# Kernel optimization log

Hardware: AMD Instinct MI355X
Metric: run time of the kernel (lower is better)

The kernel has to match this reference:

```python
import jax, jax.numpy as jnp
import numpy as np
from jax import lax

EPS = 1e-3  # Keras BatchNormalization default epsilon
DN = ('NHWC', 'HWIO', 'NHWC')


def _bn(x, gamma, beta, mean, var):
    inv = gamma * lax.rsqrt(var + EPS)
    return x * inv + (beta - mean * inv)


def setup_inputs() -> dict:
    key = jax.random.key(0)
    ks = jax.random.split(key, 5)
    B, H, W, C = 32, 56, 56, 256
    G, CG = 32, 4  # cardinality, channels per group
    CM = G * CG    # 128 mid channels
    x = jax.random.normal(ks[0], (B, H, W, C), jnp.float32)
    # 32 branch 1x1 convs (256->4 each) stacked -> one 256->128 conv
    w1 = jax.random.normal(ks[1], (1, 1, C, CM), jnp.float32) * 0.05
    b1 = jnp.zeros((CM,), jnp.float32)
    g1 = jnp.ones((CM,), jnp.float32)
    be1 = jnp.zeros((CM,), jnp.float32)
    m1 = jnp.zeros((CM,), jnp.float32)
    v1 = jnp.ones((CM,), jnp.float32)
    # 32 branch 3x3 convs (4->4 each) stacked -> grouped conv kernel [3,3,4,128]
    w2 = jax.random.normal(ks[2], (3, 3, CG, CM), jnp.float32) * 0.1
    b2 = jnp.zeros((CM,), jnp.float32)
    g2 = jnp.ones((CM,), jnp.float32)
    be2 = jnp.zeros((CM,), jnp.float32)
    m2 = jnp.zeros((CM,), jnp.float32)
    v2 = jnp.ones((CM,), jnp.float32)
    # final 1x1 conv 128 -> 256
    w3 = jax.random.normal(ks[3], (1, 1, CM, C), jnp.float32) * 0.05
    b3 = jnp.zeros((C,), jnp.float32)
    return dict(x=x, w1=w1, b1=b1, g1=g1, be1=be1, m1=m1, v1=v1,
                w2=w2, b2=b2, g2=g2, be2=be2, m2=m2, v2=v2,
                w3=w3, b3=b3)


def reference(x, w1, b1, g1, be1, m1, v1, w2, b2, g2, be2, m2, v2, w3, b3):
    # branch 1x1 convs fused: conv 256 -> 128
    h = lax.conv_general_dilated(x, w1, (1, 1), 'SAME', dimension_numbers=DN) + b1
    h = jax.nn.relu(_bn(h, g1, be1, m1, v1))
    # branch 3x3 convs fused: grouped conv, 32 groups of 4 channels
    h = lax.conv_general_dilated(h, w2, (1, 1), 'SAME', dimension_numbers=DN,
                                 feature_group_count=32) + b2
    h = jax.nn.relu(_bn(h, g2, be2, m2, v2))
    # Dropout(0.2) is identity at inference
    # final 1x1 conv 128 -> 256, residual add, relu
    out = lax.conv_general_dilated(h, w3, (1, 1), 'SAME', dimension_numbers=DN) + b3
    return jax.nn.relu(out + x)
```

## Files before the change

kernel.cpp:

```cpp
#include <hip/hip_runtime.h>
#include <stdint.h>

typedef unsigned short u16;
typedef unsigned int   u32;
typedef __attribute__((ext_vector_type(8))) short bf16x8;
typedef __attribute__((ext_vector_type(4))) float f32x4;

#define EPS 1e-3f
#define NB 32
#define HW 56
#define CI 256
#define CM 128
#define PIX (NB*HW*HW)

__device__ __forceinline__ float asf(u32 i){ union{u32 u; float f;} t; t.u=i; return t.f; }
__device__ __forceinline__ u16 f2bf(float f){
  union{float f; u32 u;} t; t.f = f;
  u32 x = t.u;
  return (u16)((x + 0x7fffu + ((x>>16)&1u)) >> 16);
}

__global__ __launch_bounds__(256) void kprep(
    const float* __restrict__ w1, const float* __restrict__ b1, const float* __restrict__ g1,
    const float* __restrict__ be1, const float* __restrict__ m1, const float* __restrict__ v1,
    const float* __restrict__ w2, const float* __restrict__ b2, const float* __restrict__ g2,
    const float* __restrict__ be2, const float* __restrict__ m2, const float* __restrict__ v2,
    const float* __restrict__ w3,
    u16* __restrict__ w1s, u16* __restrict__ w3s, u16* __restrict__ w2s,
    float* __restrict__ A1, float* __restrict__ B1,
    float* __restrict__ A2, float* __restrict__ B2){
  int i = blockIdx.x*256 + threadIdx.x;
  if (i < 32768){
    {
      int j = i & 7, lane = (i >> 3) & 63, kt = (i >> 9) & 7, t = i >> 12;
      int col = lane & 15, quad = lane >> 4;
      int n = t*16 + col, k = kt*32 + quad*8 + j;
      w1s[i] = f2bf(w1[k*CM + n]);
    }
    {
      int j = i & 7, lane = (i >> 3) & 63, kc = (i >> 9) & 3, t = i >> 11;
      int col = lane & 15, quad = lane >> 4;
      int n = t*16 + col, k = kc*32 + quad*8 + j;
      w3s[i] = f2bf(w3[k*CI + n]);
    }
  }
  if (i < 40960){
    int j = i & 7, lane = (i >> 3) & 63;
    int pv = (i >> 9) % 10, t = (i >> 9) / 10;
    int pp = pv % 5; bool lo = pv >= 5;
    int col = lane & 15, quad = lane >> 4;
    int klocal = quad*8 + j;
    int tap = (klocal < 16) ? 2*pp : 2*pp + 1;
    int c = klocal & 15;
    float wv = 0.f;
    if (tap <= 8 && (c >> 2) == (col >> 2))
      wv = w2[(tap*4 + (c & 3))*CM + t*16 + col];
    u16 hi = f2bf(wv);
    if (!lo) w2s[i] = hi;
    else     w2s[i] = f2bf(wv - asf((u32)hi << 16));
  }
  if (i < 128){
    float s1 = g1[i] * rsqrtf(v1[i] + EPS);
    A1[i] = s1;
    B1[i] = b1[i]*s1 + be1[i] - m1[i]*s1;
    float s2 = g2[i] * rsqrtf(v2[i] + EPS);
    A2[i] = s2;
    B2[i] = b2[i]*s2 + be2[i] - m2[i]*s2;
  }
}

#define K1_LS 72
__global__ __launch_bounds__(256) void k1(const float* __restrict__ x,
    const u16* __restrict__ w1s, const float* __restrict__ A1v,
    const float* __restrict__ B1v, u16* __restrict__ h1){
  __shared__ __align__(16) char smem[128*136*2];
  u16* As = (u16*)smem;
  const int tid  = threadIdx.x;
  const int lane = tid & 63, wv = tid >> 6;
  const int col  = lane & 15, quad = lane >> 4;
  const long p0 = (long)blockIdx.x * 128;
  f32x4 acc[8][2];
  #pragma unroll
  for (int a = 0; a < 8; a++)
    #pragma unroll
    for (int b = 0; b < 2; b++){ acc[a][b][0]=0.f; acc[a][b][1]=0.f; acc[a][b][2]=0.f; acc[a][b][3]=0.f; }
  for (int kc = 0; kc < 4; kc++){
    #pragma unroll
    for (int r = 0; r < 8; r++){
      int idx = r*256 + tid;
      int m = idx >> 4, f4 = idx & 15;
      float4 v = *(const float4*)(x + (p0+m)*CI + kc*64 + f4*4);
      u32 lo = (u32)f2bf(v.x) | ((u32)f2bf(v.y) << 16);
      u32 hi = (u32)f2bf(v.z) | ((u32)f2bf(v.w) << 16);
      *(uint2*)(As + m*K1_LS + f4*4) = make_uint2(lo, hi);
    }
    __syncthreads();
    #pragma unroll
    for (int ks = 0; ks < 2; ks++){
      const int kt = kc*2 + ks;
      bf16x8 bfr[2], af[8];
      #pragma unroll
      for (int nt = 0; nt < 2; nt++)
        bfr[nt] = *(const bf16x8*)(w1s + (size_t)(((wv*2+nt)*8 + kt)*64 + lane)*8);
      #pragma unroll
      for (int mt = 0; mt < 8; mt++)
        af[mt] = *(const bf16x8*)(As + (mt*16 + col)*K1_LS + ks*32 + quad*8);
      #pragma unroll
      for (int mt = 0; mt < 8; mt++)
        #pragma unroll
        for (int nt = 0; nt < 2; nt++)
          acc[mt][nt] = __builtin_amdgcn_mfma_f32_16x16x32_bf16(af[mt], bfr[nt], acc[mt][nt], 0, 0, 0);
    }
    __syncthreads();
  }
  u16* outw = (u16*)smem;
  #pragma unroll
  for (int nt = 0; nt < 2; nt++){
    int n = wv*32 + nt*16 + col;
    float a1 = A1v[n], b1v = B1v[n];
    #pragma unroll
    for (int mt = 0; mt < 8; mt++)
      #pragma unroll
      for (int reg = 0; reg < 4; reg++){
        int m = mt*16 + quad*4 + reg;
        outw[m*136 + n] = f2bf(fmaxf(acc[mt][nt][reg]*a1 + b1v, 0.f));
      }
  }
  __syncthreads();
  #pragma unroll
  for (int r = 0; r < 8; r++){
    int idx = r*256 + tid;
    int m = idx >> 4, u4 = idx & 15;
    uint4 v = *(const uint4*)(outw + m*136 + u4*8);
    *(uint4*)(h1 + (p0+m)*CM + u4*8) = v;
  }
}

#define LSH1 136
__global__ __launch_bounds__(512, 2) void k23(const u16* __restrict__ h1,
    const u16* __restrict__ w2s, const float* __restrict__ A2v,
    const float* __restrict__ B2v, const u16* __restrict__ w3s,
    const float* __restrict__ b3, const float* __restrict__ x,
    float* __restrict__ out){
  __shared__ __align__(16) char smem[3*HW*LSH1*2 + 64*256];
  u16*  tile = (u16*)smem;
  char* h2t  = smem + 3*HW*LSH1*2;
  float* pre = (float*)smem;

  const int tid = threadIdx.x;
  const int bid = blockIdx.x;
  const int blk = (bid & 7)*224 + (bid >> 3);
  const int y0 = blk % HW;
  const long p0 = (long)blk * HW;

  #pragma unroll
  for (int r = 0; r < 3; r++){
    const int yy = y0 + r - 1;
    const bool valid = (yy >= 0 && yy < HW);
    const uint4* src = (const uint4*)(h1 + (long)(blk - y0 + yy)*HW*CM);
    for (int i = tid; i < 896; i += 512){
      uint4 v = make_uint4(0u,0u,0u,0u);
      if (valid) v = src[i];
      int px = i >> 4, ch = (i & 15)*8;
      *(uint4*)(tile + (r*HW + px)*LSH1 + ch) = v;
    }
  }
  __syncthreads();

  float4 xr[4];
  #pragma unroll
  for (int it = 0; it < 4; it++){
    int i = tid + it*512;
    if (i < 1792){
      int m = i >> 5, f4 = i & 31;
      xr[it] = *(const float4*)(x + (p0+m)*CI + f4*4);
    }
  }

  const int lane = tid & 63, wv = tid >> 6;
  const int col  = lane & 15, quad = lane >> 4;

  const int mh = wv >> 2, nq = wv & 3;
  f32x4 acc2[2][2];
  #pragma unroll
  for (int a = 0; a < 2; a++)
    #pragma unroll
    for (int b = 0; b < 2; b++){ acc2[a][b][0]=0.f; acc2[a][b][1]=0.f; acc2[a][b][2]=0.f; acc2[a][b][3]=0.f; }
  #pragma unroll
  for (int pp = 0; pp < 5; pp++){
    const int tA = 2*pp, tB = (pp < 4) ? 2*pp + 1 : 8;
    const int dyA = tA/3, dxA = tA%3, dyB = tB/3, dxB = tB%3;
    const int dy = (quad < 2) ? dyA : dyB;
    const int dx = (quad < 2) ? dxA : dxB;
    bf16x8 bh[2], bl[2];
    #pragma unroll
    for (int ntl = 0; ntl < 2; ntl++){
      int nt = nq*2 + ntl;
      bh[ntl] = *(const bf16x8*)(w2s + (size_t)((nt*10 + pp)*64 + lane)*8);
      bl[ntl] = *(const bf16x8*)(w2s + (size_t)((nt*10 + 5 + pp)*64 + lane)*8);
    }
    #pragma unroll
    for (int mtl = 0; mtl < 2; mtl++){
      int px = (mh*2 + mtl)*16 + col;
      int sx = px + dx - 1;
      u32 mk = (px < HW && sx >= 0 && sx < HW) ? 0xffffffffu : 0u;
      int sxc = sx < 0 ? 0 : (sx > 55 ? 55 : sx);
      const u16* abase = tile + (dy*HW + sxc)*LSH1 + (quad & 1)*8;
      #pragma unroll
      for (int ntl = 0; ntl < 2; ntl++){
        int nt = nq*2 + ntl;
        union { bf16x8 v; u32 w[4]; } af;
        af.v = *(const bf16x8*)(abase + nt*16);
        af.w[0] &= mk; af.w[1] &= mk; af.w[2] &= mk; af.w[3] &= mk;
        acc2[mtl][ntl] = __builtin_amdgcn_mfma_f32_16x16x32_bf16(af.v, bh[ntl], acc2[mtl][ntl], 0, 0, 0);
        acc2[mtl][ntl] = __builtin_amdgcn_mfma_f32_16x16x32_bf16(af.v, bl[ntl], acc2[mtl][ntl], 0, 0, 0);
      }
    }
  }
  #pragma unroll
  for (int ntl = 0; ntl < 2; ntl++){
    int co = (nq*2 + ntl)*16 + col;
    float a2 = A2v[co], b2v = B2v[co];
    #pragma unroll
    for (int mtl = 0; mtl < 2; mtl++)
      #pragma unroll
      for (int reg = 0; reg < 4; reg++){
        int m = (mh*2 + mtl)*16 + quad*4 + reg;
        float v = acc2[mtl][ntl][reg]*a2 + b2v;
        u16 hv = (m < HW) ? f2bf(fmaxf(v, 0.f)) : (u16)0;
        *(u16*)(h2t + m*256 + ((co*2) ^ ((m & 7) << 4))) = hv;
      }
  }
  __syncthreads();

  f32x4 acc3[4][2];
  #pragma unroll
  for (int a = 0; a < 4; a++)
    #pragma unroll
    for (int b = 0; b < 2; b++){ acc3[a][b][0]=0.f; acc3[a][b][1]=0.f; acc3[a][b][2]=0.f; acc3[a][b][3]=0.f; }
  float bias[2];
  #pragma unroll
  for (int nt = 0; nt < 2; nt++) bias[nt] = b3[wv*32 + nt*16 + col];
  #pragma unroll
  for (int kc = 0; kc < 4; kc++){
    bf16x8 bfr[2];
    #pragma unroll
    for (int nt = 0; nt < 2; nt++)
      bfr[nt] = *(const bf16x8*)(w3s + (size_t)(((wv*2+nt)*4 + kc)*64 + lane)*8);
    #pragma unroll
    for (int mt = 0; mt < 4; mt++){
      int row = mt*16 + col;
      bf16x8 af = *(const bf16x8*)(h2t + row*256 + ((kc*64 + quad*16) ^ ((row & 7) << 4)));
      #pragma unroll
      for (int nt = 0; nt < 2; nt++)
        acc3[mt][nt] = __builtin_amdgcn_mfma_f32_16x16x32_bf16(af, bfr[nt], acc3[mt][nt], 0, 0, 0);
    }
  }

  if (wv < 4){
    #pragma unroll
    for (int mt = 0; mt < 4; mt++)
      #pragma unroll
      for (int nt = 0; nt < 2; nt++)
        #pragma unroll
        for (int reg = 0; reg < 4; reg++){
          int m = mt*16 + quad*4 + reg;
          pre[m*132 + (wv&3)*32 + nt*16 + col] = acc3[mt][nt][reg] + bias[nt];
        }
  }
  __syncthreads();
  #pragma unroll
  for (int it = 0; it < 4; it++){
    int i = tid + it*512;
    if (i < 1792){
      int m = i >> 5, f4 = i & 31;
      float4 pv = *(const float4*)(pre + m*132 + f4*4);
      float4 o;
      o.x = fmaxf(pv.x + xr[it].x, 0.f);
      o.y = fmaxf(pv.y + xr[it].y, 0.f);
      o.z = fmaxf(pv.z + xr[it].z, 0.f);
      o.w = fmaxf(pv.w + xr[it].w, 0.f);
      *(float4*)(out + (p0+m)*CI + f4*4) = o;
    }
  }
  __syncthreads();

  if (wv >= 4){
    #pragma unroll
    for (int mt = 0; mt < 4; mt++)
      #pragma unroll
      for (int nt = 0; nt < 2; nt++)
        #pragma unroll
        for (int reg = 0; reg < 4; reg++){
          int m = mt*16 + quad*4 + reg;
          pre[m*132 + (wv&3)*32 + nt*16 + col] = acc3[mt][nt][reg] + bias[nt];
        }
  }
  __syncthreads();
  #pragma unroll
  for (int it = 0; it < 4; it++){
    int i = tid + it*512;
    if (i < 1792){
      int m = i >> 5, f4 = i & 31;
      float4 xv = *(const float4*)(x + (p0+m)*CI + 128 + f4*4);
      float4 pv = *(const float4*)(pre + m*132 + f4*4);
      float4 o;
      o.x = fmaxf(pv.x + xv.x, 0.f);
      o.y = fmaxf(pv.y + xv.y, 0.f);
      o.z = fmaxf(pv.z + xv.z, 0.f);
      o.w = fmaxf(pv.w + xv.w, 0.f);
      *(float4*)(out + (p0+m)*CI + 128 + f4*4) = o;
    }
  }
}

extern "C" void kernel_launch(void* const* d_in, const int* in_sizes, int n_in,
                              void* d_out, int out_size, void* d_ws, size_t ws_size,
                              hipStream_t stream){
  (void)in_sizes; (void)n_in; (void)out_size; (void)ws_size;
  const float* x   = (const float*)d_in[0];
  const float* w1  = (const float*)d_in[1];
  const float* b1  = (const float*)d_in[2];
  const float* g1  = (const float*)d_in[3];
  const float* be1 = (const float*)d_in[4];
  const float* m1  = (const float*)d_in[5];
  const float* v1  = (const float*)d_in[6];
  const float* w2  = (const float*)d_in[7];
  const float* b2  = (const float*)d_in[8];
  const float* g2  = (const float*)d_in[9];
  const float* be2 = (const float*)d_in[10];
  const float* m2  = (const float*)d_in[11];
  const float* v2  = (const float*)d_in[12];
  const float* w3  = (const float*)d_in[13];
  const float* b3  = (const float*)d_in[14];

  char* ws = (char*)d_ws;
  u16* h1  = (u16*)ws;
  u16* w1s = (u16*)(ws + (size_t)PIX*CM*2);
  u16* w3s = w1s + 32768;
  float* A1 = (float*)(w3s + 32768);
  float* B1 = A1 + 128;
  float* A2 = B1 + 128;
  float* B2 = A2 + 128;
  u16* w2s = (u16*)(B2 + 128);

  kprep<<<160, 256, 0, stream>>>(w1,b1,g1,be1,m1,v1,w2,b2,g2,be2,m2,v2,w3,
                                 w1s,w3s,w2s,A1,B1,A2,B2);
  k1<<<PIX/128, 256, 0, stream>>>(x, w1s, A1, B1, h1);
  k23<<<NB*HW, 512, 0, stream>>>(h1, w2s, A2, B2, w3s, b3, x, (float*)d_out);
}
```

Baseline: 250.4 us.

## Process two image rows per block in fused grouped-conv and projection kernel

The fused 3x3-grouped-conv plus 1x1-projection kernel now handles two output rows (112 pixels) per block, loading a 4-row halo tile instead of 3 rows per single row. This cuts halo reloads of h1 and amortizes the w2/w3 weight fetches over more pixels, with MFMA tiles filling 7 full 16-row tiles instead of padding 56 to 64. LDS is reused between the input tile, h2 and the output staging buffer to fit the larger tile, which adds barriers and more accumulator registers per thread and may reduce occupancy. The early prefetch of the residual x is dropped, so x is now loaded after the GEMM.

```diff
diff --git a/kernel.cpp b/kernel.cpp
--- a/kernel.cpp
+++ b/kernel.cpp
@@ -142,22 +142,22 @@
     const float* __restrict__ B2v, const u16* __restrict__ w3s,
     const float* __restrict__ b3, const float* __restrict__ x,
     float* __restrict__ out){
-  __shared__ __align__(16) char smem[3*HW*LSH1*2 + 64*256];
+  __shared__ __align__(16) char smem[4*HW*LSH1*2];
   u16*  tile = (u16*)smem;
-  char* h2t  = smem + 3*HW*LSH1*2;
+  char* h2t  = smem;
   float* pre = (float*)smem;
 
   const int tid = threadIdx.x;
   const int bid = blockIdx.x;
-  const int blk = (bid & 7)*224 + (bid >> 3);
-  const int y0 = blk % HW;
-  const long p0 = (long)blk * HW;
-
-  #pragma unroll
-  for (int r = 0; r < 3; r++){
+  const int blk = (bid & 7)*112 + (bid >> 3);
+  const int y0 = (blk % 28) * 2;
+  const long p0 = (long)blk * 112;
+
+  #pragma unroll
+  for (int r = 0; r < 4; r++){
     const int yy = y0 + r - 1;
     const bool valid = (yy >= 0 && yy < HW);
-    const uint4* src = (const uint4*)(h1 + (long)(blk - y0 + yy)*HW*CM);
+    const uint4* src = (const uint4*)(h1 + ((long)p0 + (long)(r-1)*HW)*CM);
     for (int i = tid; i < 896; i += 512){
       uint4 v = make_uint4(0u,0u,0u,0u);
       if (valid) v = src[i];
@@ -167,75 +167,58 @@
   }
   __syncthreads();
 
-  float4 xr[4];
-  #pragma unroll
-  for (int it = 0; it < 4; it++){
-    int i = tid + it*512;
-    if (i < 1792){
-      int m = i >> 5, f4 = i & 31;
-      xr[it] = *(const float4*)(x + (p0+m)*CI + f4*4);
-    }
-  }
-
   const int lane = tid & 63, wv = tid >> 6;
   const int col  = lane & 15, quad = lane >> 4;
 
-  const int mh = wv >> 2, nq = wv & 3;
-  f32x4 acc2[2][2];
-  #pragma unroll
-  for (int a = 0; a < 2; a++)
-    #pragma unroll
-    for (int b = 0; b < 2; b++){ acc2[a][b][0]=0.f; acc2[a][b][1]=0.f; acc2[a][b][2]=0.f; acc2[a][b][3]=0.f; }
+  const int nt2 = wv;
+  f32x4 acc2[7];
+  #pragma unroll
+  for (int a = 0; a < 7; a++){ acc2[a][0]=0.f; acc2[a][1]=0.f; acc2[a][2]=0.f; acc2[a][3]=0.f; }
+  int rbase[7], xq[7];
+  #pragma unroll
+  for (int mt = 0; mt < 7; mt++){
+    int px = mt*16 + col;
+    int rr = (px >= HW) ? 1 : 0;
+    rbase[mt] = rr; xq[mt] = px - rr*HW;
+  }
   #pragma unroll
   for (int pp = 0; pp < 5; pp++){
     const int tA = 2*pp, tB = (pp < 4) ? 2*pp + 1 : 8;
-    const int dyA = tA/3, dxA = tA%3, dyB = tB/3, dxB = tB%3;
-    const int dy = (quad < 2) ? dyA : dyB;
-    const int dx = (quad < 2) ? dxA : dxB;
-    bf16x8 bh[2], bl[2];
-    #pragma unroll
-    for (int ntl = 0; ntl < 2; ntl++){
-      int nt = nq*2 + ntl;
-      bh[ntl] = *(const bf16x8*)(w2s + (size_t)((nt*10 + pp)*64 + lane)*8);
-      bl[ntl] = *(const bf16x8*)(w2s + (size_t)((nt*10 + 5 + pp)*64 + lane)*8);
-    }
-    #pragma unroll
-    for (int mtl = 0; mtl < 2; mtl++){
-      int px = (mh*2 + mtl)*16 + col;
-      int sx = px + dx - 1;
-      u32 mk = (px < HW && sx >= 0 && sx < HW) ? 0xffffffffu : 0u;
+    const int dy = (quad < 2) ? tA/3 : tB/3;
+    const int dx = (quad < 2) ? tA%3 : tB%3;
+    bf16x8 bh = *(const bf16x8*)(w2s + (size_t)((nt2*10 + pp)*64 + lane)*8);
+    bf16x8 bl = *(const bf16x8*)(w2s + (size_t)((nt2*10 + 5 + pp)*64 + lane)*8);
+    #pragma unroll
+    for (int mt = 0; mt < 7; mt++){
+      int sx = xq[mt] + dx - 1;
+      u32 mk = (sx >= 0 && sx < HW) ? 0xffffffffu : 0u;
       int sxc = sx < 0 ? 0 : (sx > 55 ? 55 : sx);
-      const u16* abase = tile + (dy*HW + sxc)*LSH1 + (quad & 1)*8;
-      #pragma unroll
-      for (int ntl = 0; ntl < 2; ntl++){
-        int nt = nq*2 + ntl;
-        union { bf16x8 v; u32 w[4]; } af;
-        af.v = *(const bf16x8*)(abase + nt*16);
-        af.w[0] &= mk; af.w[1] &= mk; af.w[2] &= mk; af.w[3] &= mk;
-        acc2[mtl][ntl] = __builtin_amdgcn_mfma_f32_16x16x32_bf16(af.v, bh[ntl], acc2[mtl][ntl], 0, 0, 0);
-        acc2[mtl][ntl] = __builtin_amdgcn_mfma_f32_16x16x32_bf16(af.v, bl[ntl], acc2[mtl][ntl], 0, 0, 0);
+      const u16* ap = tile + ((rbase[mt]+dy)*HW + sxc)*LSH1 + (quad & 1)*8 + nt2*16;
+      union { bf16x8 v; u32 w[4]; } af;
+      af.v = *(const bf16x8*)ap;
+      af.w[0] &= mk; af.w[1] &= mk; af.w[2] &= mk; af.w[3] &= mk;
+      acc2[mt] = __builtin_amdgcn_mfma_f32_16x16x32_bf16(af.v, bh, acc2[mt], 0, 0, 0);
+      acc2[mt] = __builtin_amdgcn_mfma_f32_16x16x32_bf16(af.v, bl, acc2[mt], 0, 0, 0);
+    }
+  }
+  __syncthreads();
+
+  {
+    float a2 = A2v[nt2*16 + col], b2v = B2v[nt2*16 + col];
+    #pragma unroll
+    for (int mt = 0; mt < 7; mt++)
+      #pragma unroll
+      for (int reg = 0; reg < 4; reg++){
+        int m = mt*16 + quad*4 + reg;
+        u16 hv = f2bf(fmaxf(acc2[mt][reg]*a2 + b2v, 0.f));
+        *(u16*)(h2t + m*256 + (((nt2*16 + col)*2) ^ ((m & 7) << 4))) = hv;
       }
-    }
-  }
-  #pragma unroll
-  for (int ntl = 0; ntl < 2; ntl++){
-    int co = (nq*2 + ntl)*16 + col;
-    float a2 = A2v[co], b2v = B2v[co];
-    #pragma unroll
-    for (int mtl = 0; mtl < 2; mtl++)
-      #pragma unroll
-      for (int reg = 0; reg < 4; reg++){
-        int m = (mh*2 + mtl)*16 + quad*4 + reg;
-        float v = acc2[mtl][ntl][reg]*a2 + b2v;
-        u16 hv = (m < HW) ? f2bf(fmaxf(v, 0.f)) : (u16)0;
-        *(u16*)(h2t + m*256 + ((co*2) ^ ((m & 7) << 4))) = hv;
-      }
-  }
-  __syncthreads();
-
-  f32x4 acc3[4][2];
-  #pragma unroll
-  for (int a = 0; a < 4; a++)
+  }
+  __syncthreads();
+
+  f32x4 acc3[7][2];
+  #pragma unroll
+  for (int a = 0; a < 7; a++)
     #pragma unroll
     for (int b = 0; b < 2; b++){ acc3[a][b][0]=0.f; acc3[a][b][1]=0.f; acc3[a][b][2]=0.f; acc3[a][b][3]=0.f; }
   float bias[2];
@@ -248,7 +231,7 @@
     for (int nt = 0; nt < 2; nt++)
       bfr[nt] = *(const bf16x8*)(w3s + (size_t)(((wv*2+nt)*4 + kc)*64 + lane)*8);
     #pragma unroll
-    for (int mt = 0; mt < 4; mt++){
+    for (int mt = 0; mt < 7; mt++){
       int row = mt*16 + col;
       bf16x8 af = *(const bf16x8*)(h2t + row*256 + ((kc*64 + quad*16) ^ ((row & 7) << 4)));
       #pragma unroll
@@ -256,61 +239,42 @@
         acc3[mt][nt] = __builtin_amdgcn_mfma_f32_16x16x32_bf16(af, bfr[nt], acc3[mt][nt], 0, 0, 0);
     }
   }
-
-  if (wv < 4){
-    #pragma unroll
-    for (int mt = 0; mt < 4; mt++)
-      #pragma unroll
-      for (int nt = 0; nt < 2; nt++)
+  __syncthreads();
+
+  #pragma unroll
+  for (int h = 0; h < 2; h++){
+    if ((wv >> 2) == h){
+      #pragma unroll
+      for (int mt = 0; mt < 7; mt++)
         #pragma unroll
-        for (int reg = 0; reg < 4; reg++){
-          int m = mt*16 + quad*4 + reg;
-          pre[m*132 + (wv&3)*32 + nt*16 + col] = acc3[mt][nt][reg] + bias[nt];
-        }
-  }
-  __syncthreads();
-  #pragma unroll
-  for (int it = 0; it < 4; it++){
-    int i = tid + it*512;
-    if (i < 1792){
+        for (int nt = 0; nt < 2; nt++)
+          #pragma unroll
+          for (int reg = 0; reg < 4; reg++){
+            int m = mt*16 + quad*4 + reg;
+            pre[m*132 + (wv&3)*32 + nt*16 + col] = acc3[mt][nt][reg] + bias[nt];
+          }
+    }
+    __syncthreads();
+    float4 xv[7];
+    #pragma unroll
+    for (int it = 0; it < 7; it++){
+      int i = tid + it*512;
+      int m = i >> 5, f4 = i & 31;
+      xv[it] = *(const float4*)(x + (p0+m)*CI + h*128 + f4*4);
+    }
+    #pragma unroll
+    for (int it = 0; it < 7; it++){
+      int i = tid + it*512;
       int m = i >> 5, f4 = i & 31;
       float4 pv = *(const float4*)(pre + m*132 + f4*4);
       float4 o;
-      o.x = fmaxf(pv.x + xr[it].x, 0.f);
-      o.y = fmaxf(pv.y + xr[it].y, 0.f);
-      o.z = fmaxf(pv.z + xr[it].z, 0.f);
-      o.w = fmaxf(pv.w + xr[it].w, 0.f);
-      *(float4*)(out + (p0+m)*CI + f4*4) = o;
-    }
-  }
-  __syncthreads();
-
-  if (wv >= 4){
-    #pragma unroll
-    for (int mt = 0; mt < 4; mt++)
-      #pragma unroll
-      for (int nt = 0; nt < 2; nt++)
-        #pragma unroll
-        for (int reg = 0; reg < 4; reg++){
-          int m = mt*16 + quad*4 + reg;
-          pre[m*132 + (wv&3)*32 + nt*16 + col] = acc3[mt][nt][reg] + bias[nt];
-        }
-  }
-  __syncthreads();
-  #pragma unroll
-  for (int it = 0; it < 4; it++){
-    int i = tid + it*512;
-    if (i < 1792){
-      int m = i >> 5, f4 = i & 31;
-      float4 xv = *(const float4*)(x + (p0+m)*CI + 128 + f4*4);
-      float4 pv = *(const float4*)(pre + m*132 + f4*4);
-      float4 o;
-      o.x = fmaxf(pv.x + xv.x, 0.f);
-      o.y = fmaxf(pv.y + xv.y, 0.f);
-      o.z = fmaxf(pv.z + xv.z, 0.f);
-      o.w = fmaxf(pv.w + xv.w, 0.f);
-      *(float4*)(out + (p0+m)*CI + 128 + f4*4) = o;
-    }
+      o.x = fmaxf(pv.x + xv[it].x, 0.f);
+      o.y = fmaxf(pv.y + xv[it].y, 0.f);
+      o.z = fmaxf(pv.z + xv[it].z, 0.f);
+      o.w = fmaxf(pv.w + xv[it].w, 0.f);
+      *(float4*)(out + (p0+m)*CI + h*128 + f4*4) = o;
+    }
+    if (h == 0) __syncthreads();
   }
 }
 
@@ -347,5 +311,5 @@
   kprep<<<160, 256, 0, stream>>>(w1,b1,g1,be1,m1,v1,w2,b2,g2,be2,m2,v2,w3,
                                  w1s,w3s,w2s,A1,B1,A2,B2);
   k1<<<PIX/128, 256, 0, stream>>>(x, w1s, A1, B1, h1);
-  k23<<<NB*HW, 512, 0, stream>>>(h1, w2s, A2, B2, w3s, b3, x, (float*)d_out);
-}
+  k23<<<NB*28, 512, 0, stream>>>(h1, w2s, A2, B2, w3s, b3, x, (float*)d_out);
+}
```

After: 259.0 us. 3.4% more time.

## Alias shared buffers and drop early residual prefetch to fit three blocks per CU

Applied to the files above, without the earlier changes.

Shared memory now overlaps the h2 tile and the staging buffer with the input tile region, adding a barrier after the grouped conv so the tile can be reused, and shrinks the pre buffer so only the 56 valid rows are written. The residual x prefetch, which kept sixteen float registers live across both MFMA stages, is moved to just before each epilogue. Launch bounds go from two to three blocks per CU to raise occupancy. The cost is an extra barrier, and the x loads are no longer hidden behind compute.

```diff
diff --git a/kernel.cpp b/kernel.cpp
--- a/kernel.cpp
+++ b/kernel.cpp
@@ -137,15 +137,15 @@
 }
 
 #define LSH1 136
-__global__ __launch_bounds__(512, 2) void k23(const u16* __restrict__ h1,
+__global__ __launch_bounds__(512, 3) void k23(const u16* __restrict__ h1,
     const u16* __restrict__ w2s, const float* __restrict__ A2v,
     const float* __restrict__ B2v, const u16* __restrict__ w3s,
     const float* __restrict__ b3, const float* __restrict__ x,
     float* __restrict__ out){
-  __shared__ __align__(16) char smem[3*HW*LSH1*2 + 64*256];
+  __shared__ __align__(16) char smem[45952];
   u16*  tile = (u16*)smem;
-  char* h2t  = smem + 3*HW*LSH1*2;
-  float* pre = (float*)smem;
+  char* h2t  = smem;
+  float* pre = (float*)(smem + 16384);
 
   const int tid = threadIdx.x;
   const int bid = blockIdx.x;
@@ -167,16 +167,6 @@
   }
   __syncthreads();
 
-  float4 xr[4];
-  #pragma unroll
-  for (int it = 0; it < 4; it++){
-    int i = tid + it*512;
-    if (i < 1792){
-      int m = i >> 5, f4 = i & 31;
-      xr[it] = *(const float4*)(x + (p0+m)*CI + f4*4);
-    }
-  }
-
   const int lane = tid & 63, wv = tid >> 6;
   const int col  = lane & 15, quad = lane >> 4;
 
@@ -189,9 +179,8 @@
   #pragma unroll
   for (int pp = 0; pp < 5; pp++){
     const int tA = 2*pp, tB = (pp < 4) ? 2*pp + 1 : 8;
-    const int dyA = tA/3, dxA = tA%3, dyB = tB/3, dxB = tB%3;
-    const int dy = (quad < 2) ? dyA : dyB;
-    const int dx = (quad < 2) ? dxA : dxB;
+    const int dy = (quad < 2) ? tA/3 : tB/3;
+    const int dx = (quad < 2) ? tA%3 : tB%3;
     bf16x8 bh[2], bl[2];
     #pragma unroll
     for (int ntl = 0; ntl < 2; ntl++){
@@ -217,6 +206,8 @@
       }
     }
   }
+  __syncthreads();
+
   #pragma unroll
   for (int ntl = 0; ntl < 2; ntl++){
     int co = (nq*2 + ntl)*16 + col;
@@ -265,22 +256,34 @@
         #pragma unroll
         for (int reg = 0; reg < 4; reg++){
           int m = mt*16 + quad*4 + reg;
-          pre[m*132 + (wv&3)*32 + nt*16 + col] = acc3[mt][nt][reg] + bias[nt];
+          if (m < HW)
+            pre[m*132 + (wv&3)*32 + nt*16 + col] = acc3[mt][nt][reg] + bias[nt];
         }
   }
   __syncthreads();
-  #pragma unroll
-  for (int it = 0; it < 4; it++){
-    int i = tid + it*512;
-    if (i < 1792){
-      int m = i >> 5, f4 = i & 31;
-      float4 pv = *(const float4*)(pre + m*132 + f4*4);
-      float4 o;
-      o.x = fmaxf(pv.x + xr[it].x, 0.f);
-      o.y = fmaxf(pv.y + xr[it].y, 0.f);
-      o.z = fmaxf(pv.z + xr[it].z, 0.f);
-      o.w = fmaxf(pv.w + xr[it].w, 0.f);
-      *(float4*)(out + (p0+m)*CI + f4*4) = o;
+  {
+    float4 xv[4];
+    #pragma unroll
+    for (int it = 0; it < 4; it++){
+      int i = tid + it*512;
+      if (i < 1792){
+        int m = i >> 5, f4 = i & 31;
+        xv[it] = *(const float4*)(x + (p0+m)*CI + f4*4);
+      }
+    }
+    #pragma unroll
+    for (int it = 0; it < 4; it++){
+      int i = tid + it*512;
+      if (i < 1792){
+        int m = i >> 5, f4 = i & 31;
+        float4 pv = *(const float4*)(pre + m*132 + f4*4);
+        float4 o;
+        o.x = fmaxf(pv.x + xv[it].x, 0.f);
+        o.y = fmaxf(pv.y + xv[it].y, 0.f);
+        o.z = fmaxf(pv.z + xv[it].z, 0.f);
+        o.w = fmaxf(pv.w + xv[it].w, 0.f);
+        *(float4*)(out + (p0+m)*CI + f4*4) = o;
+      }
     }
   }
   __syncthreads();
@@ -293,23 +296,34 @@
         #pragma unroll
         for (int reg = 0; reg < 4; reg++){
           int m = mt*16 + quad*4 + reg;
-          pre[m*132 + (wv&3)*32 + nt*16 + col] = acc3[mt][nt][reg] + bias[nt];
+          if (m < HW)
+            pre[m*132 + (wv&3)*32 + nt*16 + col] = acc3[mt][nt][reg] + bias[nt];
         }
   }
   __syncthreads();
-  #pragma unroll
-  for (int it = 0; it < 4; it++){
-    int i = tid + it*512;
-    if (i < 1792){
-      int m = i >> 5, f4 = i & 31;
-      float4 xv = *(const float4*)(x + (p0+m)*CI + 128 + f4*4);
-      float4 pv = *(const float4*)(pre + m*132 + f4*4);
-      float4 o;
-      o.x = fmaxf(pv.x + xv.x, 0.f);
-      o.y = fmaxf(pv.y + xv.y, 0.f);
-      o.z = fmaxf(pv.z + xv.z, 0.f);
-      o.w = fmaxf(pv.w + xv.w, 0.f);
-      *(float4*)(out + (p0+m)*CI + 128 + f4*4) = o;
+  {
+    float4 xv[4];
+    #pragma unroll
+    for (int it = 0; it < 4; it++){
+      int i = tid + it*512;
+      if (i < 1792){
+        int m = i >> 5, f4 = i & 31;
+        xv[it] = *(const float4*)(x + (p0+m)*CI + 128 + f4*4);
+      }
+    }
+    #pragma unroll
+    for (int it = 0; it < 4; it++){
+      int i = tid + it*512;
+      if (i < 1792){
+        int m = i >> 5, f4 = i & 31;
+        float4 pv = *(const float4*)(pre + m*132 + f4*4);
+        float4 o;
+        o.x = fmaxf(pv.x + xv[it].x, 0.f);
+        o.y = fmaxf(pv.y + xv[it].y, 0.f);
+        o.z = fmaxf(pv.z + xv[it].z, 0.f);
+        o.w = fmaxf(pv.w + xv[it].w, 0.f);
+        *(float4*)(out + (p0+m)*CI + 128 + f4*4) = o;
+      }
     }
   }
 }
```

After: 253.5 us. No clear change (+1.2%).

## Double k1 block to 512 threads, prefetch x chunks, use packed bf16 convert

Applied to the files above, without the earlier changes.

The 1x1 conv kernel k1 now launches 512 threads per block, so eight waves split the 128x128 output tile into 2x4 sub-tiles and each wave holds half as many accumulators. The next K chunk of x is loaded into registers while MFMAs run on the current chunk, which hides global load latency behind compute. The fp32-to-bf16 conversion now uses the hardware v_cvt_pk_bf16_f32 instruction instead of software rounding. The tradeoff is more waves contending for the same LDS tile and barriers, plus extra registers for the prefetch buffer.

```diff
diff --git a/kernel.cpp b/kernel.cpp
--- a/kernel.cpp
+++ b/kernel.cpp
@@ -18,6 +18,11 @@
   union{float f; u32 u;} t; t.f = f;
   u32 x = t.u;
   return (u16)((x + 0x7fffu + ((x>>16)&1u)) >> 16);
+}
+__device__ __forceinline__ u32 f2bf2(float lo, float hi){
+  u32 r;
+  asm("v_cvt_pk_bf16_f32 %0, %1, %2" : "=v"(r) : "v"(lo), "v"(hi));
+  return r;
 }
 
 __global__ __launch_bounds__(256) void kprep(
@@ -70,7 +75,7 @@
 }
 
 #define K1_LS 72
-__global__ __launch_bounds__(256) void k1(const float* __restrict__ x,
+__global__ __launch_bounds__(512, 2) void k1(const float* __restrict__ x,
     const u16* __restrict__ w1s, const float* __restrict__ A1v,
     const float* __restrict__ B1v, u16* __restrict__ h1){
   __shared__ __align__(16) char smem[128*136*2];
@@ -78,35 +83,51 @@
   const int tid  = threadIdx.x;
   const int lane = tid & 63, wv = tid >> 6;
   const int col  = lane & 15, quad = lane >> 4;
+  const int mh = wv >> 2, nq = wv & 3;
   const long p0 = (long)blockIdx.x * 128;
-  f32x4 acc[8][2];
-  #pragma unroll
-  for (int a = 0; a < 8; a++)
+
+  const float* xp[4];
+  int sm[4], sf[4];
+  #pragma unroll
+  for (int r = 0; r < 4; r++){
+    int idx = r*512 + tid;
+    sm[r] = idx >> 4; sf[r] = idx & 15;
+    xp[r] = x + (p0 + sm[r])*CI + sf[r]*4;
+  }
+  float4 pf[4];
+  #pragma unroll
+  for (int r = 0; r < 4; r++) pf[r] = *(const float4*)(xp[r]);
+
+  f32x4 acc[4][2];
+  #pragma unroll
+  for (int a = 0; a < 4; a++)
     #pragma unroll
     for (int b = 0; b < 2; b++){ acc[a][b][0]=0.f; acc[a][b][1]=0.f; acc[a][b][2]=0.f; acc[a][b][3]=0.f; }
+
   for (int kc = 0; kc < 4; kc++){
     #pragma unroll
-    for (int r = 0; r < 8; r++){
-      int idx = r*256 + tid;
-      int m = idx >> 4, f4 = idx & 15;
-      float4 v = *(const float4*)(x + (p0+m)*CI + kc*64 + f4*4);
-      u32 lo = (u32)f2bf(v.x) | ((u32)f2bf(v.y) << 16);
-      u32 hi = (u32)f2bf(v.z) | ((u32)f2bf(v.w) << 16);
-      *(uint2*)(As + m*K1_LS + f4*4) = make_uint2(lo, hi);
+    for (int r = 0; r < 4; r++){
+      u32 lo = f2bf2(pf[r].x, pf[r].y);
+      u32 hi = f2bf2(pf[r].z, pf[r].w);
+      *(uint2*)(As + sm[r]*K1_LS + sf[r]*4) = make_uint2(lo, hi);
     }
     __syncthreads();
+    if (kc < 3){
+      #pragma unroll
+      for (int r = 0; r < 4; r++) pf[r] = *(const float4*)(xp[r] + (kc+1)*64);
+    }
     #pragma unroll
     for (int ks = 0; ks < 2; ks++){
       const int kt = kc*2 + ks;
-      bf16x8 bfr[2], af[8];
+      bf16x8 bfr[2], af[4];
       #pragma unroll
       for (int nt = 0; nt < 2; nt++)
-        bfr[nt] = *(const bf16x8*)(w1s + (size_t)(((wv*2+nt)*8 + kt)*64 + lane)*8);
-      #pragma unroll
-      for (int mt = 0; mt < 8; mt++)
-        af[mt] = *(const bf16x8*)(As + (mt*16 + col)*K1_LS + ks*32 + quad*8);
-      #pragma unroll
-      for (int mt = 0; mt < 8; mt++)
+        bfr[nt] = *(const bf16x8*)(w1s + (size_t)(((nq*2+nt)*8 + kt)*64 + lane)*8);
+      #pragma unroll
+      for (int mt = 0; mt < 4; mt++)
+        af[mt] = *(const bf16x8*)(As + ((mh*4+mt)*16 + col)*K1_LS + ks*32 + quad*8);
+      #pragma unroll
+      for (int mt = 0; mt < 4; mt++)
         #pragma unroll
         for (int nt = 0; nt < 2; nt++)
           acc[mt][nt] = __builtin_amdgcn_mfma_f32_16x16x32_bf16(af[mt], bfr[nt], acc[mt][nt], 0, 0, 0);
@@ -116,20 +137,20 @@
   u16* outw = (u16*)smem;
   #pragma unroll
   for (int nt = 0; nt < 2; nt++){
-    int n = wv*32 + nt*16 + col;
+    int n = (nq*2+nt)*16 + col;
     float a1 = A1v[n], b1v = B1v[n];
     #pragma unroll
-    for (int mt = 0; mt < 8; mt++)
+    for (int mt = 0; mt < 4; mt++)
       #pragma unroll
       for (int reg = 0; reg < 4; reg++){
-        int m = mt*16 + quad*4 + reg;
+        int m = mh*64 + mt*16 + quad*4 + reg;
         outw[m*136 + n] = f2bf(fmaxf(acc[mt][nt][reg]*a1 + b1v, 0.f));
       }
   }
   __syncthreads();
   #pragma unroll
-  for (int r = 0; r < 8; r++){
-    int idx = r*256 + tid;
+  for (int r = 0; r < 4; r++){
+    int idx = r*512 + tid;
     int m = idx >> 4, u4 = idx & 15;
     uint4 v = *(const uint4*)(outw + m*136 + u4*8);
     *(uint4*)(h1 + (p0+m)*CM + u4*8) = v;
@@ -189,9 +210,8 @@
   #pragma unroll
   for (int pp = 0; pp < 5; pp++){
     const int tA = 2*pp, tB = (pp < 4) ? 2*pp + 1 : 8;
-    const int dyA = tA/3, dxA = tA%3, dyB = tB/3, dxB = tB%3;
-    const int dy = (quad < 2) ? dyA : dyB;
-    const int dx = (quad < 2) ? dxA : dxB;
+    const int dy = (quad < 2) ? tA/3 : tB/3;
+    const int dx = (quad < 2) ? tA%3 : tB%3;
     bf16x8 bh[2], bl[2];
     #pragma unroll
     for (int ntl = 0; ntl < 2; ntl++){
@@ -346,6 +366,6 @@
 
   kprep<<<160, 256, 0, stream>>>(w1,b1,g1,be1,m1,v1,w2,b2,g2,be2,m2,v2,w3,
                                  w1s,w3s,w2s,A1,B1,A2,B2);
-  k1<<<PIX/128, 256, 0, stream>>>(x, w1s, A1, B1, h1);
+  k1<<<PIX/128, 512, 0, stream>>>(x, w1s, A1, B1, h1);
   k23<<<NB*HW, 512, 0, stream>>>(h1, w2s, A2, B2, w3s, b3, x, (float*)d_out);
 }
```

Measured after the change: 247.9 us. No clear change (-1.0%).
